# Kernel tuning notes

Measured on AMD Instinct MI355X. Metric: run time of the kernel, lower is better.

The kernel has to match this reference:

```python
import jax, jax.numpy as jnp
import numpy as np

B, N, C, H = 8, 1024, 1024, 16
D = C // H
SCALE = D ** -0.5


def setup_inputs() -> dict:
    key = jax.random.key(0)
    ks = jax.random.split(key, 5)
    s = 0.02  # keep pre-softmax logits in a sane range
    return {
        "x": jax.random.normal(ks[0], (B, N, C), dtype=jnp.float32),
        "Wq": jax.random.normal(ks[1], (C, C), dtype=jnp.float32) * s,
        "bq": jax.random.normal(ks[2], (C,), dtype=jnp.float32) * s,
        "Wkv": jax.random.normal(ks[3], (C, 2 * C), dtype=jnp.float32) * s,
        "bkv": jax.random.normal(ks[4], (2 * C,), dtype=jnp.float32) * s,
    }


def reference(x, Wq, bq, Wkv, bkv):
    b, n, c = x.shape
    h, d = H, c // H
    q = (x @ Wq + bq).reshape(b, n, h, d)                 # [b,n,h,d]
    kv = x @ Wkv + bkv                                     # [b,n,2c]
    k, v = jnp.split(kv, 2, axis=-1)                       # each [b,n,c]
    k = k.reshape(b, n, h, d)
    v = v.reshape(b, n, h, d)
    att = jnp.einsum("bnhd,bmhd->bnmh", q, k) * SCALE      # [b,n,m,h]
    att = jax.nn.softmax(att, axis=2)                      # softmax over keys (m)
    out = jnp.einsum("bnmh,bmhd->bnhd", att, v).reshape(b, n, c)
    return out
```

## Files before the change

### kernel.cpp

```cpp
#include <hip/hip_runtime.h>
#include <stdint.h>

using u16 = unsigned short;
using u32 = unsigned int;
using bf16x8 = __attribute__((ext_vector_type(8))) __bf16;
using f32x4  = __attribute__((ext_vector_type(4))) float;

#define NB 8
#define NN 1024
#define NC 1024
#define NH 16
#define ND 64
#define QSCALE 0.18033688011112042f

__device__ __forceinline__ u16 f2bf(float f) {
  u32 u = __float_as_uint(f);
  return (u16)((u + 0x7fffu + ((u >> 16) & 1u)) >> 16);
}
__device__ __forceinline__ u16 bfc(float f) {
  __bf16 b = (__bf16)f;
  return __builtin_bit_cast(u16, b);
}
__device__ __forceinline__ u32 pack2(u16 a, u16 b) { return (u32)a | ((u32)b << 16); }

__device__ __forceinline__ void gload16(const void* g, void* l) {
  __builtin_amdgcn_global_load_lds((__attribute__((address_space(1))) const u32*)g,
                                   (__attribute__((address_space(3))) u32*)l, 16, 0, 0);
}

__global__ void k_prep(const float* __restrict__ x, const float* __restrict__ Wq,
                       const float* __restrict__ Wkv,
                       u16* __restrict__ xb, u16* __restrict__ Wt) {
  __shared__ u16 tile[64][72];
  int bid = blockIdx.x;
  int t = threadIdx.x;
  if (bid < 8192) {
    int i = bid * 256 + t;
    float4 v = ((const float4*)x)[i];
    ((uint2*)xb)[i] = make_uint2(pack2(f2bf(v.x), f2bf(v.y)), pack2(f2bf(v.z), f2bf(v.w)));
    return;
  }
  {
    int pb = bid - 8192;
    int k0 = (pb & 15) << 6;
    int c0 = (pb >> 4) << 6;
    bool isQ = (c0 < 1024);
    const float* src = isQ ? Wq : Wkv;
    int ldw  = isQ ? 1024 : 2048;
    int csrc = isQ ? c0 : (c0 - 1024);
    float sc = isQ ? QSCALE : 1.0f;

    int r  = t >> 2;
    int cq = (t & 3) << 4;
    const float* p = src + (size_t)(k0 + r) * ldw + csrc + cq;
#pragma unroll
    for (int j = 0; j < 16; j += 4) {
      float4 v = *(const float4*)(p + j);
      tile[r][cq + j + 0] = f2bf(v.x * sc);
      tile[r][cq + j + 1] = f2bf(v.y * sc);
      tile[r][cq + j + 2] = f2bf(v.z * sc);
      tile[r][cq + j + 3] = f2bf(v.w * sc);
    }
    __syncthreads();
    int co = t >> 2;
    int kq = (t & 3) << 4;
    u16 v0[16];
#pragma unroll
    for (int j = 0; j < 16; ++j) v0[j] = tile[kq + j][co];
    uint4 o0, o1;
    o0.x = pack2(v0[0], v0[1]);  o0.y = pack2(v0[2], v0[3]);
    o0.z = pack2(v0[4], v0[5]);  o0.w = pack2(v0[6], v0[7]);
    o1.x = pack2(v0[8], v0[9]);  o1.y = pack2(v0[10], v0[11]);
    o1.z = pack2(v0[12], v0[13]); o1.w = pack2(v0[14], v0[15]);
    u16* dst = Wt + (size_t)(c0 + co) * 1024 + k0 + kq;
    *(uint4*)dst = o0;
    *(uint4*)(dst + 8) = o1;
  }
}

__launch_bounds__(512, 2)
__global__ void k_gemm(const u16* __restrict__ A, const u16* __restrict__ Bw,
                       const float* __restrict__ bq, const float* __restrict__ bkv,
                       u16* __restrict__ qws, u16* __restrict__ kws, u16* __restrict__ vtw) {
  __shared__ __align__(16) u16 LA[2][16384];
  __shared__ __align__(16) u16 LB[2][12288];
  int flat = blockIdx.x;
  int xcd = flat & 7, idx = flat >> 3;
  int m0 = (xcd * 4 + (idx & 3)) * 256;
  int n0 = (idx >> 2) * 192;
  int tid = threadIdx.x;
  int w = tid >> 6, lane = tid & 63;
  int lo = lane & 15, hi = lane >> 4;
  int wm = w >> 2, wn = w & 3;

  f32x4 acc[8][3] = {};

  int cs = ((tid & 7) ^ ((tid >> 3) & 7)) * 8;
  const u16* Ag = A  + (size_t)(m0 + (tid >> 3)) * 1024 + cs;
  const u16* Bg = Bw + (size_t)(n0 + (tid >> 3)) * 1024 + cs;

  int ck0 = ((hi ^ (lo & 7)) << 3);
  int ck1 = (((4 + hi) ^ (lo & 7)) << 3);
  const u16* laR = &LA[0][wm * 8192 + lo * 64];
  const u16* lbR = &LB[0][(wn * 48 + lo) * 64];

#define MFMA_(a, b, c) __builtin_amdgcn_mfma_f32_16x16x32_bf16(a, b, c, 0, 0, 0)
#define SBAR() __builtin_amdgcn_sched_barrier(0); __builtin_amdgcn_s_barrier(); __builtin_amdgcn_sched_barrier(0)
#define LGKM0() asm volatile("s_waitcnt lgkmcnt(0)" ::: "memory"); __builtin_amdgcn_sched_barrier(0)

#define ST_AH(BUF, MH, KT)                                                                     \
  gload16(Ag + (size_t)((MH) * 128) * 1024 + (KT) * 64,      &LA[BUF][(MH) * 8192 + tid * 8]); \
  gload16(Ag + (size_t)((MH) * 128 + 64) * 1024 + (KT) * 64, &LA[BUF][(MH) * 8192 + 4096 + tid * 8]);
#define ST_BT(BUF, NH, KT)                                                                     \
  gload16(Bg + (size_t)((NH) * 64) * 1024 + (KT) * 64,       &LB[BUF][(NH) * 4096 + tid * 8]);

#define QUAD(Q, NI)                                                           \
  __builtin_amdgcn_s_setprio(1);                                              \
  _Pragma("unroll")                                                           \
  for (int ks = 0; ks < 2; ++ks)                                              \
    _Pragma("unroll")                                                         \
    for (int mi = 0; mi < 4; ++mi)                                            \
      acc[(Q) * 4 + mi][NI] = MFMA_(af[mi][ks], bfr[NI][ks], acc[(Q) * 4 + mi][NI]); \
  __builtin_amdgcn_s_setprio(0);

  ST_AH(0, 0, 0); ST_AH(0, 1, 0); ST_BT(0, 0, 0); ST_BT(0, 1, 0); ST_BT(0, 2, 0);
  ST_AH(1, 0, 1); ST_AH(1, 1, 1); ST_BT(1, 0, 1); ST_BT(1, 1, 1); ST_BT(1, 2, 1);
  asm volatile("s_waitcnt vmcnt(7)" ::: "memory");
  __builtin_amdgcn_s_barrier();

#pragma unroll 1
  for (int t = 0; t < 16; ++t) {
    int b = t & 1;
    const u16* la = laR + b * 16384;
    const u16* lb = lbR + b * 12288;
    bf16x8 af[4][2], bfr[3][2];
    bool st = (t < 14);

#pragma unroll
    for (int mi = 0; mi < 4; ++mi) {
      af[mi][0] = *(const bf16x8*)(la + mi * 1024 + ck0);
      af[mi][1] = *(const bf16x8*)(la + mi * 1024 + ck1);
    }
    bfr[0][0] = *(const bf16x8*)(lb + ck0);
    bfr[0][1] = *(const bf16x8*)(lb + ck1);
    SBAR();
    LGKM0();
    QUAD(0, 0);
    SBAR();

    bfr[1][0] = *(const bf16x8*)(lb + 1024 + ck0);
    bfr[1][1] = *(const bf16x8*)(lb + 1024 + ck1);
    SBAR();
    LGKM0();
    QUAD(0, 1);
    SBAR();

    bfr[2][0] = *(const bf16x8*)(lb + 2048 + ck0);
    bfr[2][1] = *(const bf16x8*)(lb + 2048 + ck1);
    SBAR();
    LGKM0();
    QUAD(0, 2);
    SBAR();

#pragma unroll
    for (int mi = 0; mi < 4; ++mi) {
      af[mi][0] = *(const bf16x8*)(la + (4 + mi) * 1024 + ck0);
      af[mi][1] = *(const bf16x8*)(la + (4 + mi) * 1024 + ck1);
    }
    if (st) { ST_BT(b, 0, t + 2); }
    SBAR();
    LGKM0();
    QUAD(1, 0);
    SBAR();

    if (st) { ST_AH(b, 0, t + 2); ST_BT(b, 1, t + 2); }
    SBAR();
    QUAD(1, 1);
    SBAR();

    if (st) { ST_AH(b, 1, t + 2); ST_BT(b, 2, t + 2); }
    SBAR();
    QUAD(1, 2);
    if (t < 14)       { asm volatile("s_waitcnt vmcnt(7)" ::: "memory"); }
    else if (t == 14) { asm volatile("s_waitcnt vmcnt(0)" ::: "memory"); }
    SBAR();
  }
#undef QUAD
#undef ST_AH
#undef ST_BT
#undef SBAR
#undef LGKM0
#undef MFMA_

#pragma unroll
  for (int ni = 0; ni < 3; ++ni) {
    int c = n0 + wn * 48 + ni * 16 + lo;
    float bvl = (c < 1024) ? bq[c] * QSCALE : bkv[c - 1024];
    if (c < 2048) {
#pragma unroll
      for (int mi = 0; mi < 8; ++mi) {
#pragma unroll
        for (int r = 0; r < 4; ++r) {
          int m = m0 + wm * 128 + mi * 16 + hi * 4 + r;
          int b = m >> 10, tok = m & 1023;
          u16 o = f2bf(acc[mi][ni][r] + bvl);
          if (c < 1024) {
            int h = c >> 6, d = c & 63;
            qws[((size_t)(b * 16 + h) * 1024 + tok) * 64 + d] = o;
          } else {
            int c2 = c - 1024; int h = c2 >> 6, d = c2 & 63;
            kws[((size_t)(b * 16 + h) * 1024 + tok) * 64 + d] = o;
          }
        }
      }
    } else {
      int c2 = c - 2048; int h = c2 >> 6, d = c2 & 63;
#pragma unroll
      for (int mi = 0; mi < 8; ++mi) {
        int m = m0 + wm * 128 + mi * 16 + hi * 4;
        int b = m >> 10, tok = m & 1023;
        ushort4 pk;
        pk.x = bfc(acc[mi][ni][0] + bvl);
        pk.y = bfc(acc[mi][ni][1] + bvl);
        pk.z = bfc(acc[mi][ni][2] + bvl);
        pk.w = bfc(acc[mi][ni][3] + bvl);
        *(ushort4*)&vtw[((size_t)(b * 16 + h) * 64 + d) * 1024 + tok] = pk;
      }
    }
  }
}

__launch_bounds__(512)
__global__ void k_attn(const u16* __restrict__ q, const u16* __restrict__ k,
                       const u16* __restrict__ vt, float* __restrict__ out) {
  __shared__ __align__(16) u16 Ks[2][4096];
  __shared__ __align__(16) u16 Vs[2][4096];
  __shared__ __align__(16) u16 P[8][16][72];
  int bh = blockIdx.x;
  int q0 = blockIdx.y * 128;
  int tid = threadIdx.x;
  int w = tid >> 6, lane = tid & 63;
  int lo = lane & 15, hi = lane >> 4;
  int b = bh >> 4, h = bh & 15;

  const u16* kbase = k  + (size_t)bh * 65536;
  const u16* vbase = vt + (size_t)bh * 65536;

  int srow = w * 8 + (lane >> 3);
  int cg   = (lane & 7) ^ ((lane >> 3) & 7);
  const u16* gK = kbase + (size_t)srow * 64   + cg * 8;
  const u16* gV = vbase + (size_t)srow * 1024 + cg * 8;
  u16* lK0 = &Ks[0][w * 512];
  u16* lK1 = &Ks[1][w * 512];
  u16* lV0 = &Vs[0][w * 512];
  u16* lV1 = &Vs[1][w * 512];

  const u16* qp = q + ((size_t)bh * 1024 + q0 + w * 16 + lo) * 64 + hi * 8;
  bf16x8 qf0 = *(const bf16x8*)(qp);
  bf16x8 qf1 = *(const bf16x8*)(qp + 32);

  f32x4 acc_o[4] = {};
  float m_s = -1e30f;
  float l_s = 0.f;

  int sw = lo & 7;

  gload16(gK, lK0);
  gload16(gV, lV0);
  __syncthreads();

  for (int t = 0; t < 16; ++t) {
    int cur = t & 1;
    if (t < 15) {
      gload16(gK + (t + 1) * 4096, cur ? lK0 : lK1);
      gload16(gV + (t + 1) * 64,   cur ? lV0 : lV1);
    }
    f32x4 s[4] = {};
    const u16* kb = Ks[cur];
    __builtin_amdgcn_s_setprio(1);
#pragma unroll
    for (int ni = 0; ni < 4; ++ni) {
      const u16* kp = kb + (ni * 16 + lo) * 64;
      bf16x8 kf0 = *(const bf16x8*)(kp + ((hi ^ sw) * 8));
      bf16x8 kf1 = *(const bf16x8*)(kp + (((4 + hi) ^ sw) * 8));
      s[ni] = __builtin_amdgcn_mfma_f32_16x16x32_bf16(kf0, qf0, s[ni], 0, 0, 0);
      s[ni] = __builtin_amdgcn_mfma_f32_16x16x32_bf16(kf1, qf1, s[ni], 0, 0, 0);
    }
    __builtin_amdgcn_s_setprio(0);
    float pm;
    {
      float a0 = fmaxf(fmaxf(s[0][0], s[0][1]), fmaxf(s[0][2], s[0][3]));
      float a1 = fmaxf(fmaxf(s[1][0], s[1][1]), fmaxf(s[1][2], s[1][3]));
      float a2 = fmaxf(fmaxf(s[2][0], s[2][1]), fmaxf(s[2][2], s[2][3]));
      float a3 = fmaxf(fmaxf(s[3][0], s[3][1]), fmaxf(s[3][2], s[3][3]));
      pm = fmaxf(fmaxf(a0, a1), fmaxf(a2, a3));
      pm = fmaxf(pm, __shfl_xor(pm, 16));
      pm = fmaxf(pm, __shfl_xor(pm, 32));
    }
    if (!__all(pm <= m_s + 8.0f)) {
      float mn = fmaxf(m_s, pm);
      float corr = __builtin_amdgcn_exp2f(m_s - mn);
      m_s = mn;
      l_s *= corr;
      float cr[4];
#pragma unroll
      for (int r = 0; r < 4; ++r) cr[r] = __shfl(corr, hi * 4 + r);
#pragma unroll
      for (int ci = 0; ci < 4; ++ci)
#pragma unroll
        for (int r = 0; r < 4; ++r) acc_o[ci][r] *= cr[r];
    }
    float rs = 0.f;
#pragma unroll
    for (int ni = 0; ni < 4; ++ni) {
      float p0 = __builtin_amdgcn_exp2f(s[ni][0] - m_s);
      float p1 = __builtin_amdgcn_exp2f(s[ni][1] - m_s);
      float p2 = __builtin_amdgcn_exp2f(s[ni][2] - m_s);
      float p3 = __builtin_amdgcn_exp2f(s[ni][3] - m_s);
      rs += (p0 + p1) + (p2 + p3);
      ushort4 pk;
      pk.x = bfc(p0); pk.y = bfc(p1); pk.z = bfc(p2); pk.w = bfc(p3);
      *(ushort4*)&P[w][lo][ni * 16 + hi * 4] = pk;
    }
    rs += __shfl_xor(rs, 16);
    rs += __shfl_xor(rs, 32);
    l_s += rs;
    bf16x8 pf0 = *(const bf16x8*)(&P[w][lo][hi * 8]);
    bf16x8 pf1 = *(const bf16x8*)(&P[w][lo][32 + hi * 8]);
    const u16* vb = Vs[cur];
    __builtin_amdgcn_s_setprio(1);
#pragma unroll
    for (int ci = 0; ci < 4; ++ci) {
      const u16* vp = vb + (ci * 16 + lo) * 64;
      bf16x8 vf0 = *(const bf16x8*)(vp + ((hi ^ sw) * 8));
      bf16x8 vf1 = *(const bf16x8*)(vp + (((4 + hi) ^ sw) * 8));
      acc_o[ci] = __builtin_amdgcn_mfma_f32_16x16x32_bf16(pf0, vf0, acc_o[ci], 0, 0, 0);
      acc_o[ci] = __builtin_amdgcn_mfma_f32_16x16x32_bf16(pf1, vf1, acc_o[ci], 0, 0, 0);
    }
    __builtin_amdgcn_s_setprio(0);
    __syncthreads();
  }
  float inv = 1.0f / l_s;
  float ivr[4];
#pragma unroll
  for (int r = 0; r < 4; ++r) ivr[r] = __shfl(inv, hi * 4 + r);
#pragma unroll
  for (int r = 0; r < 4; ++r) {
    int n = q0 + w * 16 + hi * 4 + r;
    float* dst = out + ((size_t)(b * 1024 + n)) * 1024 + h * 64;
#pragma unroll
    for (int ci = 0; ci < 4; ++ci) dst[ci * 16 + lo] = acc_o[ci][r] * ivr[r];
  }
}

extern "C" void kernel_launch(void* const* d_in, const int* in_sizes, int n_in,
                              void* d_out, int out_size, void* d_ws, size_t ws_size,
                              hipStream_t stream) {
  const float* x   = (const float*)d_in[0];
  const float* Wq  = (const float*)d_in[1];
  const float* bq  = (const float*)d_in[2];
  const float* Wkv = (const float*)d_in[3];
  const float* bkv = (const float*)d_in[4];
  float* out = (float*)d_out;

  char* ws = (char*)d_ws;
  u16*   xb   = (u16*)(ws);
  u16*   Wt   = (u16*)(ws + 16777216);
  u16*   qws  = (u16*)(ws + 23080960);
  u16*   kws  = (u16*)(ws + 39858176);
  u16*   vtw  = (u16*)(ws + 73412608);

  k_prep<<<8960, 256, 0, stream>>>(x, Wq, Wkv, xb, Wt);
  k_gemm<<<512, 512, 0, stream>>>(xb, Wt, bq, bkv, qws, kws, vtw);
  {
    dim3 g(128, 8);
    k_attn<<<g, 512, 0, stream>>>(qws, kws, vtw, out);
  }
}
```

Baseline: 137.1 us.

## Process two 128-query tiles per attention block to reuse K/V loads

Each attention workgroup now handles 256 queries, two independent 16-row tiles per wave, instead of 128. Every K and V tile loaded into LDS and every K/V fragment read from LDS feeds twice as many MFMAs. This halves global K/V traffic and the number of barriers per query. In exchange the grid shrinks to 512 blocks, which may underfill the GPU's CUs, and per-thread register and LDS use grows.

```diff
diff --git a/kernel.cpp b/kernel.cpp
--- a/kernel.cpp
+++ b/kernel.cpp
@@ -235,9 +235,9 @@
                        const u16* __restrict__ vt, float* __restrict__ out) {
   __shared__ __align__(16) u16 Ks[2][4096];
   __shared__ __align__(16) u16 Vs[2][4096];
-  __shared__ __align__(16) u16 P[8][16][72];
+  __shared__ __align__(16) u16 P[2][8][16][72];
   int bh = blockIdx.x;
-  int q0 = blockIdx.y * 128;
+  int q0 = blockIdx.y * 256;
   int tid = threadIdx.x;
   int w = tid >> 6, lane = tid & 63;
   int lo = lane & 15, hi = lane >> 4;
@@ -256,12 +256,14 @@
   u16* lV1 = &Vs[1][w * 512];
 
   const u16* qp = q + ((size_t)bh * 1024 + q0 + w * 16 + lo) * 64 + hi * 8;
-  bf16x8 qf0 = *(const bf16x8*)(qp);
-  bf16x8 qf1 = *(const bf16x8*)(qp + 32);
-
-  f32x4 acc_o[4] = {};
-  float m_s = -1e30f;
-  float l_s = 0.f;
+  bf16x8 qfA0 = *(const bf16x8*)(qp);
+  bf16x8 qfA1 = *(const bf16x8*)(qp + 32);
+  bf16x8 qfB0 = *(const bf16x8*)(qp + 128 * 64);
+  bf16x8 qfB1 = *(const bf16x8*)(qp + 128 * 64 + 32);
+
+  f32x4 accA[4] = {}, accB[4] = {};
+  float mA = -1e30f, lA = 0.f;
+  float mB = -1e30f, lB = 0.f;
 
   int sw = lo & 7;
 
@@ -275,7 +277,7 @@
       gload16(gK + (t + 1) * 4096, cur ? lK0 : lK1);
       gload16(gV + (t + 1) * 64,   cur ? lV0 : lV1);
     }
-    f32x4 s[4] = {};
+    f32x4 sA[4] = {}, sB[4] = {};
     const u16* kb = Ks[cur];
     __builtin_amdgcn_s_setprio(1);
 #pragma unroll
@@ -283,50 +285,61 @@
       const u16* kp = kb + (ni * 16 + lo) * 64;
       bf16x8 kf0 = *(const bf16x8*)(kp + ((hi ^ sw) * 8));
       bf16x8 kf1 = *(const bf16x8*)(kp + (((4 + hi) ^ sw) * 8));
-      s[ni] = __builtin_amdgcn_mfma_f32_16x16x32_bf16(kf0, qf0, s[ni], 0, 0, 0);
-      s[ni] = __builtin_amdgcn_mfma_f32_16x16x32_bf16(kf1, qf1, s[ni], 0, 0, 0);
+      sA[ni] = __builtin_amdgcn_mfma_f32_16x16x32_bf16(kf0, qfA0, sA[ni], 0, 0, 0);
+      sA[ni] = __builtin_amdgcn_mfma_f32_16x16x32_bf16(kf1, qfA1, sA[ni], 0, 0, 0);
+      sB[ni] = __builtin_amdgcn_mfma_f32_16x16x32_bf16(kf0, qfB0, sB[ni], 0, 0, 0);
+      sB[ni] = __builtin_amdgcn_mfma_f32_16x16x32_bf16(kf1, qfB1, sB[ni], 0, 0, 0);
     }
     __builtin_amdgcn_s_setprio(0);
-    float pm;
-    {
-      float a0 = fmaxf(fmaxf(s[0][0], s[0][1]), fmaxf(s[0][2], s[0][3]));
-      float a1 = fmaxf(fmaxf(s[1][0], s[1][1]), fmaxf(s[1][2], s[1][3]));
-      float a2 = fmaxf(fmaxf(s[2][0], s[2][1]), fmaxf(s[2][2], s[2][3]));
-      float a3 = fmaxf(fmaxf(s[3][0], s[3][1]), fmaxf(s[3][2], s[3][3]));
-      pm = fmaxf(fmaxf(a0, a1), fmaxf(a2, a3));
-      pm = fmaxf(pm, __shfl_xor(pm, 16));
-      pm = fmaxf(pm, __shfl_xor(pm, 32));
-    }
-    if (!__all(pm <= m_s + 8.0f)) {
-      float mn = fmaxf(m_s, pm);
-      float corr = __builtin_amdgcn_exp2f(m_s - mn);
-      m_s = mn;
-      l_s *= corr;
-      float cr[4];
-#pragma unroll
-      for (int r = 0; r < 4; ++r) cr[r] = __shfl(corr, hi * 4 + r);
-#pragma unroll
-      for (int ci = 0; ci < 4; ++ci)
-#pragma unroll
-        for (int r = 0; r < 4; ++r) acc_o[ci][r] *= cr[r];
-    }
-    float rs = 0.f;
-#pragma unroll
-    for (int ni = 0; ni < 4; ++ni) {
-      float p0 = __builtin_amdgcn_exp2f(s[ni][0] - m_s);
-      float p1 = __builtin_amdgcn_exp2f(s[ni][1] - m_s);
-      float p2 = __builtin_amdgcn_exp2f(s[ni][2] - m_s);
-      float p3 = __builtin_amdgcn_exp2f(s[ni][3] - m_s);
-      rs += (p0 + p1) + (p2 + p3);
-      ushort4 pk;
-      pk.x = bfc(p0); pk.y = bfc(p1); pk.z = bfc(p2); pk.w = bfc(p3);
-      *(ushort4*)&P[w][lo][ni * 16 + hi * 4] = pk;
-    }
-    rs += __shfl_xor(rs, 16);
-    rs += __shfl_xor(rs, 32);
-    l_s += rs;
-    bf16x8 pf0 = *(const bf16x8*)(&P[w][lo][hi * 8]);
-    bf16x8 pf1 = *(const bf16x8*)(&P[w][lo][32 + hi * 8]);
+
+#define SOFTMAX(S, M, L, PI)                                                   \
+    {                                                                          \
+      float a0 = fmaxf(fmaxf(S[0][0], S[0][1]), fmaxf(S[0][2], S[0][3]));      \
+      float a1 = fmaxf(fmaxf(S[1][0], S[1][1]), fmaxf(S[1][2], S[1][3]));      \
+      float a2 = fmaxf(fmaxf(S[2][0], S[2][1]), fmaxf(S[2][2], S[2][3]));      \
+      float a3 = fmaxf(fmaxf(S[3][0], S[3][1]), fmaxf(S[3][2], S[3][3]));      \
+      float pm = fmaxf(fmaxf(a0, a1), fmaxf(a2, a3));                          \
+      pm = fmaxf(pm, __shfl_xor(pm, 16));                                      \
+      pm = fmaxf(pm, __shfl_xor(pm, 32));                                      \
+      if (!__all(pm <= M + 8.0f)) {                                            \
+        float mn = fmaxf(M, pm);                                               \
+        float corr = __builtin_amdgcn_exp2f(M - mn);                           \
+        M = mn;                                                                \
+        L *= corr;                                                             \
+        float cr[4];                                                           \
+        _Pragma("unroll")                                                      \
+        for (int r = 0; r < 4; ++r) cr[r] = __shfl(corr, hi * 4 + r);          \
+        _Pragma("unroll")                                                      \
+        for (int ci = 0; ci < 4; ++ci)                                         \
+          _Pragma("unroll")                                                    \
+          for (int r = 0; r < 4; ++r) acc##PI[ci][r] *= cr[r];                 \
+      }                                                                        \
+      float rs = 0.f;                                                          \
+      _Pragma("unroll")                                                        \
+      for (int ni = 0; ni < 4; ++ni) {                                         \
+        float p0 = __builtin_amdgcn_exp2f(S[ni][0] - M);                       \
+        float p1 = __builtin_amdgcn_exp2f(S[ni][1] - M);                       \
+        float p2 = __builtin_amdgcn_exp2f(S[ni][2] - M);                       \
+        float p3 = __builtin_amdgcn_exp2f(S[ni][3] - M);                       \
+        rs += (p0 + p1) + (p2 + p3);                                           \
+        ushort4 pk;                                                            \
+        pk.x = bfc(p0); pk.y = bfc(p1); pk.z = bfc(p2); pk.w = bfc(p3);        \
+        *(ushort4*)&P[PI##I][w][lo][ni * 16 + hi * 4] = pk;                    \
+      }                                                                        \
+      rs += __shfl_xor(rs, 16);                                                \
+      rs += __shfl_xor(rs, 32);                                                \
+      L += rs;                                                                 \
+    }
+#define AI 0
+#define BI 1
+    SOFTMAX(sA, mA, lA, A)
+    SOFTMAX(sB, mB, lB, B)
+#undef SOFTMAX
+
+    bf16x8 pA0 = *(const bf16x8*)(&P[0][w][lo][hi * 8]);
+    bf16x8 pA1 = *(const bf16x8*)(&P[0][w][lo][32 + hi * 8]);
+    bf16x8 pB0 = *(const bf16x8*)(&P[1][w][lo][hi * 8]);
+    bf16x8 pB1 = *(const bf16x8*)(&P[1][w][lo][32 + hi * 8]);
     const u16* vb = Vs[cur];
     __builtin_amdgcn_s_setprio(1);
 #pragma unroll
@@ -334,22 +347,39 @@
       const u16* vp = vb + (ci * 16 + lo) * 64;
       bf16x8 vf0 = *(const bf16x8*)(vp + ((hi ^ sw) * 8));
       bf16x8 vf1 = *(const bf16x8*)(vp + (((4 + hi) ^ sw) * 8));
-      acc_o[ci] = __builtin_amdgcn_mfma_f32_16x16x32_bf16(pf0, vf0, acc_o[ci], 0, 0, 0);
-      acc_o[ci] = __builtin_amdgcn_mfma_f32_16x16x32_bf16(pf1, vf1, acc_o[ci], 0, 0, 0);
+      accA[ci] = __builtin_amdgcn_mfma_f32_16x16x32_bf16(pA0, vf0, accA[ci], 0, 0, 0);
+      accA[ci] = __builtin_amdgcn_mfma_f32_16x16x32_bf16(pA1, vf1, accA[ci], 0, 0, 0);
+      accB[ci] = __builtin_amdgcn_mfma_f32_16x16x32_bf16(pB0, vf0, accB[ci], 0, 0, 0);
+      accB[ci] = __builtin_amdgcn_mfma_f32_16x16x32_bf16(pB1, vf1, accB[ci], 0, 0, 0);
     }
     __builtin_amdgcn_s_setprio(0);
     __syncthreads();
   }
-  float inv = 1.0f / l_s;
-  float ivr[4];
-#pragma unroll
-  for (int r = 0; r < 4; ++r) ivr[r] = __shfl(inv, hi * 4 + r);
-#pragma unroll
-  for (int r = 0; r < 4; ++r) {
-    int n = q0 + w * 16 + hi * 4 + r;
-    float* dst = out + ((size_t)(b * 1024 + n)) * 1024 + h * 64;
-#pragma unroll
-    for (int ci = 0; ci < 4; ++ci) dst[ci * 16 + lo] = acc_o[ci][r] * ivr[r];
+  {
+    float inv = 1.0f / lA;
+    float ivr[4];
+#pragma unroll
+    for (int r = 0; r < 4; ++r) ivr[r] = __shfl(inv, hi * 4 + r);
+#pragma unroll
+    for (int r = 0; r < 4; ++r) {
+      int n = q0 + w * 16 + hi * 4 + r;
+      float* dst = out + ((size_t)(b * 1024 + n)) * 1024 + h * 64;
+#pragma unroll
+      for (int ci = 0; ci < 4; ++ci) dst[ci * 16 + lo] = accA[ci][r] * ivr[r];
+    }
+  }
+  {
+    float inv = 1.0f / lB;
+    float ivr[4];
+#pragma unroll
+    for (int r = 0; r < 4; ++r) ivr[r] = __shfl(inv, hi * 4 + r);
+#pragma unroll
+    for (int r = 0; r < 4; ++r) {
+      int n = q0 + 128 + w * 16 + hi * 4 + r;
+      float* dst = out + ((size_t)(b * 1024 + n)) * 1024 + h * 64;
+#pragma unroll
+      for (int ci = 0; ci < 4; ++ci) dst[ci * 16 + lo] = accB[ci][r] * ivr[r];
+    }
   }
 }
 
@@ -373,7 +403,7 @@
   k_prep<<<8960, 256, 0, stream>>>(x, Wq, Wkv, xb, Wt);
   k_gemm<<<512, 512, 0, stream>>>(xb, Wt, bq, bkv, qws, kws, vtw);
   {
-    dim3 g(128, 8);
+    dim3 g(128, 4);
     k_attn<<<g, 512, 0, stream>>>(qws, kws, vtw, out);
   }
 }
```

New measurement: 132.5 us. 1.03x faster.
